# Optimization experiments

Hardware: AMD Instinct MI355X
Metric: run time of the kernel (lower is better)

Reference implementation:

```python
import jax, jax.numpy as jnp
import numpy as np

H = 256      # hidden_dim
NH = 8       # num_heads
D = H // NH  # per-head dim
NEG = -(2.0**32) + 1.0
EPS = 1e-5


def setup_inputs() -> dict:
    key = jax.random.key(0)
    ks = jax.random.split(key, 12)
    N, Tq, Tk = 2, 2048, 2048
    s = 1.0 / np.sqrt(H)
    return {
        "Q": jax.random.normal(ks[0], (N, Tq, H), jnp.float32),
        "K": jax.random.normal(ks[1], (N, Tk, H), jnp.float32),
        "V": jax.random.normal(ks[2], (N, Tk, H), jnp.float32),
        "Wq": jax.random.normal(ks[3], (H, H), jnp.float32) * s,
        "bq": jnp.zeros((H,), jnp.float32),
        "Wk": jax.random.normal(ks[4], (H, H), jnp.float32) * s,
        "bk": jnp.zeros((H,), jnp.float32),
        "Wv": jax.random.normal(ks[5], (H, H), jnp.float32) * s,
        "bv": jnp.zeros((H,), jnp.float32),
        "gamma": jnp.ones((H,), jnp.float32),
        "beta": jnp.zeros((H,), jnp.float32),
    }


def _split_heads(x):
    # [N,T,H] -> [h,N,T,D]  (matches torch split(dim=2)+cat(dim=0): head-major)
    N, T, _ = x.shape
    return x.reshape(N, T, NH, D).transpose(2, 0, 1, 3)


def reference(Q, K, V, Wq, bq, Wk, bk, Wv, bv, gamma, beta):
    N, Tq, _ = Q.shape
    Tk = K.shape[1]
    Ql = jax.nn.relu(Q @ Wq + bq)
    Kl = jax.nn.relu(K @ Wk + bk)
    Vl = jax.nn.relu(V @ Wv + bv)
    Qh, Kh, Vh = _split_heads(Ql), _split_heads(Kl), _split_heads(Vl)

    scores = jnp.einsum("hnqd,hnkd->hnqk", Qh, Kh) / jnp.sqrt(jnp.float32(D))
    key_mask = jnp.sign(jnp.abs(K).sum(-1))    # [N,Tk]
    scores = jnp.where(key_mask[None, :, None, :] == 0, NEG, scores)
    attn = jax.nn.softmax(scores / 0.01, axis=-1)
    query_mask = jnp.sign(jnp.abs(Q).sum(-1))  # [N,Tq]
    attn = attn * query_mask[None, :, :, None]  # dropout p=0 -> identity

    ctx = jnp.einsum("hnqk,hnkd->hnqd", attn[..., :-1], Vh[:, :, :-1, :])
    out = ctx.transpose(1, 2, 0, 3).reshape(N, Tq, H)

    mu = out.mean(-1, keepdims=True)
    var = ((out - mu) ** 2).mean(-1, keepdims=True)
    out = (out - mu) / jnp.sqrt(var + EPS) * gamma + beta

    weight = attn.transpose(1, 2, 0, 3).reshape(N, Tq, NH * Tk).mean(-1)
    return out, weight
```

## Files before the change

kernel.cpp:

```cpp
#include <hip/hip_runtime.h>
#include <math.h>

#define H_DIM 256
#define NHEAD 8
#define DHEAD 32
#define NB 2
#define TSEQ 2048
#define LN_EPS 1e-5f

#define QK2_SCALE 25.503486f
#define SPLIT 4
#define TILES_PER (TSEQ / 64 / SPLIT)

typedef _Float16 half8 __attribute__((ext_vector_type(8)));
typedef _Float16 half4t __attribute__((ext_vector_type(4)));
typedef _Float16 half2t __attribute__((ext_vector_type(2)));
typedef float f32x4 __attribute__((ext_vector_type(4)));

__device__ __forceinline__ f32x4 mfma16(half8 a, half8 b, f32x4 c) {
  return __builtin_amdgcn_mfma_f32_16x16x32_f16(a, b, c, 0, 0, 0);
}
__device__ __forceinline__ float exp2fast(float x) {
  return __builtin_amdgcn_exp2f(x);
}
__device__ __forceinline__ half2t pkrtz(float a, float b) {
  return __builtin_bit_cast(half2t, __builtin_amdgcn_cvt_pkrtz(a, b));
}

__global__ __launch_bounds__(256) void mask_kernel(
    const float* __restrict__ Q, const float* __restrict__ K,
    float* __restrict__ qmask, float* __restrict__ kmask) {
  const int wid = threadIdx.x >> 6, lane = threadIdx.x & 63;
  int row = blockIdx.x * 4 + wid;
  const int total_q = NB * TSEQ;
  const float* src;
  float* dst;
  if (row < total_q) { src = Q + (size_t)row * H_DIM; dst = qmask + row; }
  else               { src = K + (size_t)(row - total_q) * H_DIM; dst = kmask + (row - total_q); }
  float4 v = *(const float4*)(src + lane * 4);
  float s = fabsf(v.x) + fabsf(v.y) + fabsf(v.z) + fabsf(v.w);
  #pragma unroll
  for (int off = 32; off > 0; off >>= 1) s += __shfl_xor(s, off);
  if (lane == 0) *dst = (s != 0.0f) ? 1.0f : 0.0f;
}

__global__ __launch_bounds__(256) void prepack_kernel(
    const float* __restrict__ Wq, const float* __restrict__ Wk, const float* __restrict__ Wv,
    const float* __restrict__ kmask,
    half8* __restrict__ WpkHi, half8* __restrict__ WpkLo, half8* __restrict__ AmaskF) {
  if (blockIdx.x >= 96) {
    int slot2 = (blockIdx.x - 96) * 256 + threadIdx.x;
    int n = slot2 >> 12;
    int rem = slot2 & 4095;
    int tile = rem >> 7;
    int c = (rem >> 6) & 1;
    int lane = rem & 63;
    int quad = lane >> 4, l15 = lane & 15;
    half8 am;
    #pragma unroll
    for (int j = 0; j < 8; ++j)
      am[j] = (l15 == 0) ? (_Float16)kmask[(size_t)n * TSEQ + tile * 64 + c * 32 + quad * 8 + j]
                         : (_Float16)0.0f;
    AmaskF[(((size_t)n * 32 + tile) * 2 + c) * 64 + lane] = am;
    return;
  }
  int slot = blockIdx.x * 256 + threadIdx.x;
  int lane = slot & 63;
  int fg = (slot >> 6) & 15;
  int s  = (slot >> 10) & 7;
  int which = slot >> 13;
  const float* W = which == 0 ? Wq : which == 1 ? Wk : Wv;
  int j  = fg * 16 + (lane & 15);
  int kb = s * 32 + (lane >> 4) * 8;
  half8 hi, lo;
  #pragma unroll
  for (int jj = 0; jj < 8; ++jj) {
    float x = W[(size_t)(kb + jj) * H_DIM + j];
    _Float16 h = (_Float16)x;
    hi[jj] = h;
    lo[jj] = (_Float16)(x - (float)h);
  }
  WpkHi[slot] = hi;
  WpkLo[slot] = lo;
}

__global__ __launch_bounds__(256) void proj_kernel(
    const float* __restrict__ Q, const float* __restrict__ K, const float* __restrict__ V,
    const float* __restrict__ bq, const float* __restrict__ bk, const float* __restrict__ bv,
    const half8* __restrict__ WpkHi, const half8* __restrict__ WpkLo,
    const float* __restrict__ kmask,
    half8* __restrict__ Gqhi, half8* __restrict__ Gqlo,
    half8* __restrict__ Gkhi, half8* __restrict__ Gklo, half8* __restrict__ Gv) {
  const int which = blockIdx.z;
  const float* X    = which == 0 ? Q  : which == 1 ? K  : V;
  const float* bias = which == 0 ? bq : which == 1 ? bk : bv;

  __shared__ __align__(16) float T[64 * 68];

  const int tid = threadIdx.x;
  const int w = tid >> 6, lane = tid & 63;
  const int l15 = lane & 15, quad = lane >> 4;
  const int mbase = blockIdx.y * 64;
  const int nfg   = blockIdx.x * 4;
  const int nn   = mbase >> 11;
  const int tile = blockIdx.y & 31;

  half8 ahi[8], alo[8];
  {
    const float* xrow = X + (size_t)(mbase + w * 16 + l15) * H_DIM + quad * 8;
    #pragma unroll
    for (int s = 0; s < 8; ++s) {
      float4 a0 = *(const float4*)(xrow + s * 32);
      float4 a1 = *(const float4*)(xrow + s * 32 + 4);
      float xs[8] = {a0.x, a0.y, a0.z, a0.w, a1.x, a1.y, a1.z, a1.w};
      #pragma unroll
      for (int i = 0; i < 8; ++i) {
        _Float16 h = (_Float16)xs[i];
        ahi[s][i] = h;
        alo[s][i] = (_Float16)(xs[i] - (float)h);
      }
    }
  }

  f32x4 acc[4];
  #pragma unroll
  for (int f = 0; f < 4; ++f) acc[f] = (f32x4){0.f, 0.f, 0.f, 0.f};

  #pragma unroll
  for (int s = 0; s < 8; ++s) {
    const half8* ph = WpkHi + (((size_t)which * 8 + s) * 16 + nfg) * 64 + lane;
    const half8* pl = WpkLo + (((size_t)which * 8 + s) * 16 + nfg) * 64 + lane;
    #pragma unroll
    for (int f = 0; f < 4; ++f) {
      half8 BH = ph[f * 64];
      half8 BL = pl[f * 64];
      acc[f] = mfma16(ahi[s], BH, acc[f]);
      acc[f] = mfma16(ahi[s], BL, acc[f]);
      acc[f] = mfma16(alo[s], BH, acc[f]);
    }
  }

  #pragma unroll
  for (int f = 0; f < 4; ++f) {
    float bj = bias[blockIdx.x * 64 + f * 16 + l15];
    #pragma unroll
    for (int r = 0; r < 4; ++r) {
      int row = w * 16 + quad * 4 + r;
      float val = fmaxf(acc[f][r] + bj, 0.0f);
      if (which == 2 && ((mbase + row) & (TSEQ - 1)) == TSEQ - 1) val = 0.0f;
      T[row * 68 + f * 16 + l15] = val;
    }
  }
  __syncthreads();

  if (which < 2) {
    const int fq = tid >> 6, lp = tid & 63;
    const int kdc = lp >> 4, krlo = lp & 15;
    const int row = fq * 16 + krlo;
    const float sc = (which == 0) ? QK2_SCALE : 1.0f;
    #pragma unroll
    for (int hs = 0; hs < 2; ++hs) {
      const float* p = &T[row * 68 + hs * 32 + kdc * 8];
      float4 a0 = *(const float4*)p;
      float4 a1 = *(const float4*)(p + 4);
      float xs[8] = {a0.x, a0.y, a0.z, a0.w, a1.x, a1.y, a1.z, a1.w};
      half8 hi, lo;
      #pragma unroll
      for (int i = 0; i < 8; ++i) {
        float x = xs[i] * sc;
        _Float16 h = (_Float16)x;
        hi[i] = h;
        lo[i] = (_Float16)(x - (float)h);
      }
      int hn = (blockIdx.x * 2 + hs) * NB + nn;
      size_t di = ((size_t)hn * 32 + tile) * 256 + tid;
      if (which == 0) { Gqhi[di] = hi; Gqlo[di] = lo; }
      else            { Gkhi[di] = hi; Gklo[di] = lo; }
    }
  } else {
    const int top = tid >> 6, mid = (tid >> 4) & 3, low = tid & 15;
    const int c = top >> 1, hh = top & 1;
    const int trow0 = (c * 4 + mid) * 8;
    float km[8];
    #pragma unroll
    for (int j = 0; j < 8; ++j)
      km[j] = kmask[(size_t)nn * TSEQ + tile * 64 + trow0 + j];
    #pragma unroll
    for (int hs = 0; hs < 2; ++hs) {
      const int col = hs * 32 + hh * 16 + low;
      half8 v8;
      #pragma unroll
      for (int j = 0; j < 8; ++j)
        v8[j] = (_Float16)(T[(trow0 + j) * 68 + col] * km[j]);
      int hn = (blockIdx.x * 2 + hs) * NB + nn;
      Gv[((size_t)hn * 32 + tile) * 256 + tid] = v8;
    }
  }
}

__global__ __launch_bounds__(256) void attn_kernel(
    const half8* __restrict__ Gqhi, const half8* __restrict__ Gqlo,
    const half8* __restrict__ Gkhi, const half8* __restrict__ Gklo,
    const half8* __restrict__ Gv, const half8* __restrict__ AmaskF,
    _Float16* __restrict__ Opf, float* __restrict__ Mp, float* __restrict__ Lp) {
  __shared__ __align__(16) half8 Vf[2][256];
  __shared__ __align__(16) _Float16 Pbuf[4][16][72];

  const int tid = threadIdx.x;
  const int w = tid >> 6, lane = tid & 63;
  const int l15 = lane & 15, quad = lane >> 4;

  const int b = blockIdx.x;
  const int g    = ((b & 7) << 1) | ((b >> 3) & 1);
  const int qt   = (b >> 4) & 31;
  const int sblk = b >> 9;
  const int n = g & 1;

  const size_t fbase = (size_t)g * 32 * 256;
  const int tile0 = sblk * TILES_PER;

  half8 qhi = Gqhi[fbase + (size_t)qt * 256 + w * 64 + lane];
  half8 qlo = Gqlo[fbase + (size_t)qt * 256 + w * 64 + lane];

  float m_q = -1.0e30f;
  f32x4 O0, O1, Ol;
  O0 = (f32x4){0.f, 0.f, 0.f, 0.f};
  O1 = (f32x4){0.f, 0.f, 0.f, 0.f};
  Ol = (f32x4){0.f, 0.f, 0.f, 0.f};

  const half8* kh  = Gkhi + fbase + (size_t)tile0 * 256 + lane;
  const half8* kl  = Gklo + fbase + (size_t)tile0 * 256 + lane;
  const half8* gv  = Gv   + fbase + (size_t)tile0 * 256 + tid;
  const half8* amp = AmaskF + (((size_t)n * 32 + tile0) * 2) * 64 + lane;

  half8 KH[4], KL[4];
  #pragma unroll
  for (int f = 0; f < 4; ++f) { KH[f] = kh[f * 64]; KL[f] = kl[f * 64]; }
  Vf[0][tid] = gv[0];

  #pragma unroll
  for (int tt = 0; tt < TILES_PER; ++tt) {
    half8 KHn[4], KLn[4], vnext;
    if (tt < TILES_PER - 1) {
      #pragma unroll
      for (int f = 0; f < 4; ++f) { KHn[f] = kh[256 + f * 64]; KLn[f] = kl[256 + f * 64]; }
      vnext = gv[256];
    }
    half8 am0 = amp[0];
    half8 am1 = amp[64];

    __syncthreads();
    if (tt < TILES_PER - 1)
      Vf[(tt + 1) & 1][tid] = vnext;

    f32x4 S[4];
    #pragma unroll
    for (int f = 0; f < 4; ++f) {
      f32x4 a = (f32x4){0.f, 0.f, 0.f, 0.f};
      a = mfma16(KL[f], qhi, a);
      a = mfma16(KH[f], qlo, a);
      a = mfma16(KH[f], qhi, a);
      S[f] = a;
    }

    float t0 = fmaxf(fmaxf(S[0][0], S[0][1]), fmaxf(S[0][2], S[0][3]));
    float t1 = fmaxf(fmaxf(S[1][0], S[1][1]), fmaxf(S[1][2], S[1][3]));
    float t2 = fmaxf(fmaxf(S[2][0], S[2][1]), fmaxf(S[2][2], S[2][3]));
    float t3 = fmaxf(fmaxf(S[3][0], S[3][1]), fmaxf(S[3][2], S[3][3]));
    float mx = fmaxf(fmaxf(t0, t1), fmaxf(t2, t3));
    mx = fmaxf(mx, __shfl_xor(mx, 16));
    mx = fmaxf(mx, __shfl_xor(mx, 32));

    float mnew = fmaxf(m_q, mx);
    float alpha = exp2fast(m_q - mnew);
    m_q = mnew;

    #pragma unroll
    for (int f = 0; f < 4; ++f) {
      float p0 = exp2fast(S[f][0] - m_q);
      float p1 = exp2fast(S[f][1] - m_q);
      float p2 = exp2fast(S[f][2] - m_q);
      float p3 = exp2fast(S[f][3] - m_q);
      half2t a01 = pkrtz(p0, p1);
      half2t a23 = pkrtz(p2, p3);
      *(half2t*)&Pbuf[w][l15][f * 16 + quad * 4]     = a01;
      *(half2t*)&Pbuf[w][l15][f * 16 + quad * 4 + 2] = a23;
    }
    #pragma unroll
    for (int r = 0; r < 4; ++r) { O0[r] *= alpha; O1[r] *= alpha; }
    Ol[0] *= alpha;
    asm volatile("s_waitcnt lgkmcnt(0)" ::: "memory");

    const half8* vbuf = (const half8*)Vf[tt & 1];
    #pragma unroll
    for (int c = 0; c < 2; ++c) {
      half8 pb = *(const half8*)&Pbuf[w][l15][c * 32 + quad * 8];
      O0 = mfma16(vbuf[(c * 2 + 0) * 64 + lane], pb, O0);
      O1 = mfma16(vbuf[(c * 2 + 1) * 64 + lane], pb, O1);
      Ol = mfma16(c == 0 ? am0 : am1, pb, Ol);
    }

    #pragma unroll
    for (int f = 0; f < 4; ++f) { KH[f] = KHn[f]; KL[f] = KLn[f]; }
    kh += 256; kl += 256; gv += 256; amp += 128;
  }

  {
    int q = qt * 64 + w * 16 + l15;
    size_t idx = ((size_t)(sblk * 16 + g) * TSEQ + q) * DHEAD;
    half4t o0 = {(_Float16)O0[0], (_Float16)O0[1], (_Float16)O0[2], (_Float16)O0[3]};
    half4t o1 = {(_Float16)O1[0], (_Float16)O1[1], (_Float16)O1[2], (_Float16)O1[3]};
    *(half4t*)&Opf[idx + quad * 4]      = o0;
    *(half4t*)&Opf[idx + 16 + quad * 4] = o1;
    if (quad == 0) {
      Mp[(size_t)(sblk * 16 + g) * TSEQ + q] = m_q;
      Lp[(size_t)(sblk * 16 + g) * TSEQ + q] = Ol[0];
    }
  }
}

__global__ __launch_bounds__(256) void ln_kernel(
    const _Float16* __restrict__ Opf, const float* __restrict__ Mp, const float* __restrict__ Lp,
    const float* __restrict__ gamma, const float* __restrict__ beta,
    const float* __restrict__ qmask,
    float* __restrict__ out, float* __restrict__ wout) {
  const int wid = threadIdx.x >> 6, lane = threadIdx.x & 63;
  const int row = blockIdx.x * 4 + wid;
  const int n = row >> 11, q = row & (TSEQ - 1);
  const int hh = lane >> 3;
  const int hn = hh * NB + n;
  const int dbase = (lane & 7) * 4;

  float m[SPLIT], l[SPLIT];
  half4t P[SPLIT];
  #pragma unroll
  for (int i = 0; i < SPLIT; ++i) {
    size_t si = (size_t)(i * 16 + hn) * TSEQ + q;
    P[i] = *(const half4t*)&Opf[si * DHEAD + dbase];
    m[i] = Mp[si];
    l[i] = Lp[si];
  }
  float mm = fmaxf(fmaxf(m[0], m[1]), fmaxf(m[2], m[3]));
  float denom = 0.f;
  float a[SPLIT];
  #pragma unroll
  for (int i = 0; i < SPLIT; ++i) { a[i] = exp2fast(m[i] - mm); denom += l[i] * a[i]; }
  float qm = qmask[row];
  float inv = qm / denom;

  float4 x = make_float4(0.f, 0.f, 0.f, 0.f);
  #pragma unroll
  for (int i = 0; i < SPLIT; ++i) {
    x.x += (float)P[i][0] * a[i]; x.y += (float)P[i][1] * a[i];
    x.z += (float)P[i][2] * a[i]; x.w += (float)P[i][3] * a[i];
  }
  x.x *= inv; x.y *= inv; x.z *= inv; x.w *= inv;

  float s = x.x + x.y + x.z + x.w;
  #pragma unroll
  for (int off = 32; off > 0; off >>= 1) s += __shfl_xor(s, off);
  float mu = s * (1.0f / H_DIM);
  float dx0 = x.x - mu, dx1 = x.y - mu, dx2 = x.z - mu, dx3 = x.w - mu;
  float sq = dx0 * dx0 + dx1 * dx1 + dx2 * dx2 + dx3 * dx3;
  #pragma unroll
  for (int off = 32; off > 0; off >>= 1) sq += __shfl_xor(sq, off);
  float rstd = rsqrtf(sq * (1.0f / H_DIM) + LN_EPS);
  float4 g = *(const float4*)(gamma + lane * 4);
  float4 bb = *(const float4*)(beta + lane * 4);
  float4 y;
  y.x = dx0 * rstd * g.x + bb.x;
  y.y = dx1 * rstd * g.y + bb.y;
  y.z = dx2 * rstd * g.z + bb.z;
  y.w = dx3 * rstd * g.w + bb.w;
  *(float4*)(out + (size_t)row * H_DIM + lane * 4) = y;
  if (lane == 0) wout[row] = qm * (1.0f / TSEQ);
}

extern "C" void kernel_launch(void* const* d_in, const int* in_sizes, int n_in,
                              void* d_out, int out_size, void* d_ws, size_t ws_size,
                              hipStream_t stream) {
  const float* Q  = (const float*)d_in[0];
  const float* K  = (const float*)d_in[1];
  const float* V  = (const float*)d_in[2];
  const float* Wq = (const float*)d_in[3];
  const float* bq = (const float*)d_in[4];
  const float* Wk = (const float*)d_in[5];
  const float* bk = (const float*)d_in[6];
  const float* Wv = (const float*)d_in[7];
  const float* bv = (const float*)d_in[8];
  const float* gamma = (const float*)d_in[9];
  const float* beta  = (const float*)d_in[10];

  char* ws = (char*)d_ws;
  const size_t NFRAG = (size_t)16 * 32 * 256;
  _Float16* Opf = (_Float16*)ws;
  half8* Gqhi = (half8*)(ws + (size_t)SPLIT * 16 * TSEQ * DHEAD * 2);
  half8* Gqlo = Gqhi + NFRAG;
  half8* Gkhi = Gqlo + NFRAG;
  half8* Gklo = Gkhi + NFRAG;
  half8* Gv   = Gklo + NFRAG;
  float* Mp = (float*)(Gv + NFRAG);
  float* Lp = Mp + SPLIT * 16 * TSEQ;
  float* qmask = Lp + SPLIT * 16 * TSEQ;
  float* kmask = qmask + NB * TSEQ;
  half8* WpkHi = (half8*)(kmask + NB * TSEQ);
  half8* WpkLo = WpkHi + 24576;
  half8* AmaskF = WpkLo + 24576;

  float* out  = (float*)d_out;
  float* wout = out + (size_t)NB * TSEQ * H_DIM;

  hipLaunchKernelGGL(mask_kernel, dim3(2 * NB * TSEQ / 4), dim3(256), 0, stream,
                     Q, K, qmask, kmask);
  hipLaunchKernelGGL(prepack_kernel, dim3(128), dim3(256), 0, stream,
                     Wq, Wk, Wv, kmask, WpkHi, WpkLo, AmaskF);
  hipLaunchKernelGGL(proj_kernel, dim3(H_DIM / 64, NB * TSEQ / 64, 3), dim3(256), 0, stream,
                     Q, K, V, bq, bk, bv, WpkHi, WpkLo, kmask,
                     Gqhi, Gqlo, Gkhi, Gklo, Gv);
  hipLaunchKernelGGL(attn_kernel, dim3(16 * 32 * SPLIT), dim3(256), 0, stream,
                     Gqhi, Gqlo, Gkhi, Gklo, Gv, AmaskF, Opf, Mp, Lp);
  hipLaunchKernelGGL(ln_kernel, dim3(NB * TSEQ / 4), dim3(256), 0, stream,
                     Opf, Mp, Lp, gamma, beta, qmask, out, wout);
}
```

Before: 131.5 us.

## Stage K/V/mask tiles through shared memory and fuse setup kernels

In the attention kernel, each wave used to load the K hi/lo fragments directly from global memory, and all four waves fetched the same data. Now the block cooperatively loads K hi/lo, V and the mask fragment into double-buffered shared memory, with one sync per tile, so each global fetch is shared. The mask and weight-prepack kernels are merged into one setup kernel, and the AmaskF construction moves into the K projection blocks, which removes a launch. It also adds a launch-bounds occupancy hint and a single packed half4 store for P. The trade-off is more LDS reads per tile and a larger shared-memory footprint.

Result: faster. 127.0 us (-3.4%).

```diff
diff --git a/kernel.cpp b/kernel.cpp
--- a/kernel.cpp
+++ b/kernel.cpp
@@ -27,44 +27,28 @@
   return __builtin_bit_cast(half2t, __builtin_amdgcn_cvt_pkrtz(a, b));
 }
 
-__global__ __launch_bounds__(256) void mask_kernel(
+__global__ __launch_bounds__(256) void setup_kernel(
     const float* __restrict__ Q, const float* __restrict__ K,
-    float* __restrict__ qmask, float* __restrict__ kmask) {
-  const int wid = threadIdx.x >> 6, lane = threadIdx.x & 63;
-  int row = blockIdx.x * 4 + wid;
-  const int total_q = NB * TSEQ;
-  const float* src;
-  float* dst;
-  if (row < total_q) { src = Q + (size_t)row * H_DIM; dst = qmask + row; }
-  else               { src = K + (size_t)(row - total_q) * H_DIM; dst = kmask + (row - total_q); }
-  float4 v = *(const float4*)(src + lane * 4);
-  float s = fabsf(v.x) + fabsf(v.y) + fabsf(v.z) + fabsf(v.w);
-  #pragma unroll
-  for (int off = 32; off > 0; off >>= 1) s += __shfl_xor(s, off);
-  if (lane == 0) *dst = (s != 0.0f) ? 1.0f : 0.0f;
-}
-
-__global__ __launch_bounds__(256) void prepack_kernel(
     const float* __restrict__ Wq, const float* __restrict__ Wk, const float* __restrict__ Wv,
-    const float* __restrict__ kmask,
-    half8* __restrict__ WpkHi, half8* __restrict__ WpkLo, half8* __restrict__ AmaskF) {
-  if (blockIdx.x >= 96) {
-    int slot2 = (blockIdx.x - 96) * 256 + threadIdx.x;
-    int n = slot2 >> 12;
-    int rem = slot2 & 4095;
-    int tile = rem >> 7;
-    int c = (rem >> 6) & 1;
-    int lane = rem & 63;
-    int quad = lane >> 4, l15 = lane & 15;
-    half8 am;
-    #pragma unroll
-    for (int j = 0; j < 8; ++j)
-      am[j] = (l15 == 0) ? (_Float16)kmask[(size_t)n * TSEQ + tile * 64 + c * 32 + quad * 8 + j]
-                         : (_Float16)0.0f;
-    AmaskF[(((size_t)n * 32 + tile) * 2 + c) * 64 + lane] = am;
+    float* __restrict__ qmask, float* __restrict__ kmask,
+    half8* __restrict__ WpkHi, half8* __restrict__ WpkLo) {
+  const int tid = threadIdx.x;
+  if (blockIdx.x < 2048) {
+    const int wid = tid >> 6, lane = tid & 63;
+    int row = blockIdx.x * 4 + wid;
+    const int total_q = NB * TSEQ;
+    const float* src;
+    float* dst;
+    if (row < total_q) { src = Q + (size_t)row * H_DIM; dst = qmask + row; }
+    else               { src = K + (size_t)(row - total_q) * H_DIM; dst = kmask + (row - total_q); }
+    float4 v = *(const float4*)(src + lane * 4);
+    float s = fabsf(v.x) + fabsf(v.y) + fabsf(v.z) + fabsf(v.w);
+    #pragma unroll
+    for (int off = 32; off > 0; off >>= 1) s += __shfl_xor(s, off);
+    if (lane == 0) *dst = (s != 0.0f) ? 1.0f : 0.0f;
     return;
   }
-  int slot = blockIdx.x * 256 + threadIdx.x;
+  int slot = (blockIdx.x - 2048) * 256 + tid;
   int lane = slot & 63;
   int fg = (slot >> 6) & 15;
   int s  = (slot >> 10) & 7;
@@ -90,7 +74,8 @@
     const half8* __restrict__ WpkHi, const half8* __restrict__ WpkLo,
     const float* __restrict__ kmask,
     half8* __restrict__ Gqhi, half8* __restrict__ Gqlo,
-    half8* __restrict__ Gkhi, half8* __restrict__ Gklo, half8* __restrict__ Gv) {
+    half8* __restrict__ Gkhi, half8* __restrict__ Gklo, half8* __restrict__ Gv,
+    half8* __restrict__ AmaskF) {
   const int which = blockIdx.z;
   const float* X    = which == 0 ? Q  : which == 1 ? K  : V;
   const float* bias = which == 0 ? bq : which == 1 ? bk : bv;
@@ -177,6 +162,16 @@
       if (which == 0) { Gqhi[di] = hi; Gqlo[di] = lo; }
       else            { Gkhi[di] = hi; Gklo[di] = lo; }
     }
+    if (which == 1 && blockIdx.x == 0 && tid < 128) {
+      int c = tid >> 6, lane2 = tid & 63;
+      int quad2 = lane2 >> 4, l15b = lane2 & 15;
+      half8 am;
+      #pragma unroll
+      for (int j = 0; j < 8; ++j)
+        am[j] = (l15b == 0) ? (_Float16)kmask[(size_t)nn * TSEQ + tile * 64 + c * 32 + quad2 * 8 + j]
+                            : (_Float16)0.0f;
+      AmaskF[(((size_t)nn * 32 + tile) * 2 + c) * 64 + lane2] = am;
+    }
   } else {
     const int top = tid >> 6, mid = (tid >> 4) & 3, low = tid & 15;
     const int c = top >> 1, hh = top & 1;
@@ -198,12 +193,15 @@
   }
 }
 
-__global__ __launch_bounds__(256) void attn_kernel(
+__global__ __launch_bounds__(256, 4) void attn_kernel(
     const half8* __restrict__ Gqhi, const half8* __restrict__ Gqlo,
     const half8* __restrict__ Gkhi, const half8* __restrict__ Gklo,
     const half8* __restrict__ Gv, const half8* __restrict__ AmaskF,
     _Float16* __restrict__ Opf, float* __restrict__ Mp, float* __restrict__ Lp) {
-  __shared__ __align__(16) half8 Vf[2][256];
+  __shared__ __align__(16) half8 KhB[2][256];
+  __shared__ __align__(16) half8 KlB[2][256];
+  __shared__ __align__(16) half8 VB[2][256];
+  __shared__ __align__(16) half8 AB[2][128];
   __shared__ __align__(16) _Float16 Pbuf[4][16][72];
 
   const int tid = threadIdx.x;
@@ -228,38 +226,37 @@
   O1 = (f32x4){0.f, 0.f, 0.f, 0.f};
   Ol = (f32x4){0.f, 0.f, 0.f, 0.f};
 
-  const half8* kh  = Gkhi + fbase + (size_t)tile0 * 256 + lane;
-  const half8* kl  = Gklo + fbase + (size_t)tile0 * 256 + lane;
-  const half8* gv  = Gv   + fbase + (size_t)tile0 * 256 + tid;
-  const half8* amp = AmaskF + (((size_t)n * 32 + tile0) * 2) * 64 + lane;
-
-  half8 KH[4], KL[4];
-  #pragma unroll
-  for (int f = 0; f < 4; ++f) { KH[f] = kh[f * 64]; KL[f] = kl[f * 64]; }
-  Vf[0][tid] = gv[0];
+  const half8* gkh = Gkhi + fbase + (size_t)tile0 * 256;
+  const half8* gkl = Gklo + fbase + (size_t)tile0 * 256;
+  const half8* gvv = Gv   + fbase + (size_t)tile0 * 256;
+  const half8* gam = AmaskF + (size_t)(n * 32 + tile0) * 128;
+
+  KhB[0][tid] = gkh[tid];
+  KlB[0][tid] = gkl[tid];
+  VB[0][tid]  = gvv[tid];
+  if (tid < 128) AB[0][tid] = gam[tid];
+  __syncthreads();
 
   #pragma unroll
   for (int tt = 0; tt < TILES_PER; ++tt) {
-    half8 KHn[4], KLn[4], vnext;
+    const int cur = tt & 1, nxt = cur ^ 1;
+    half8 rkh, rkl, rv, ra;
     if (tt < TILES_PER - 1) {
-      #pragma unroll
-      for (int f = 0; f < 4; ++f) { KHn[f] = kh[256 + f * 64]; KLn[f] = kl[256 + f * 64]; }
-      vnext = gv[256];
-    }
-    half8 am0 = amp[0];
-    half8 am1 = amp[64];
-
-    __syncthreads();
-    if (tt < TILES_PER - 1)
-      Vf[(tt + 1) & 1][tid] = vnext;
+      rkh = gkh[(tt + 1) * 256 + tid];
+      rkl = gkl[(tt + 1) * 256 + tid];
+      rv  = gvv[(tt + 1) * 256 + tid];
+      if (tid < 128) ra = gam[(tt + 1) * 128 + tid];
+    }
 
     f32x4 S[4];
     #pragma unroll
     for (int f = 0; f < 4; ++f) {
+      half8 KH = KhB[cur][f * 64 + lane];
+      half8 KL = KlB[cur][f * 64 + lane];
       f32x4 a = (f32x4){0.f, 0.f, 0.f, 0.f};
-      a = mfma16(KL[f], qhi, a);
-      a = mfma16(KH[f], qlo, a);
-      a = mfma16(KH[f], qhi, a);
+      a = mfma16(KL, qhi, a);
+      a = mfma16(KH, qlo, a);
+      a = mfma16(KH, qhi, a);
       S[f] = a;
     }
 
@@ -283,15 +280,18 @@
       float p3 = exp2fast(S[f][3] - m_q);
       half2t a01 = pkrtz(p0, p1);
       half2t a23 = pkrtz(p2, p3);
-      *(half2t*)&Pbuf[w][l15][f * 16 + quad * 4]     = a01;
-      *(half2t*)&Pbuf[w][l15][f * 16 + quad * 4 + 2] = a23;
+      half4t pk4;
+      pk4[0] = a01[0]; pk4[1] = a01[1]; pk4[2] = a23[0]; pk4[3] = a23[1];
+      *(half4t*)&Pbuf[w][l15][f * 16 + quad * 4] = pk4;
     }
     #pragma unroll
     for (int r = 0; r < 4; ++r) { O0[r] *= alpha; O1[r] *= alpha; }
     Ol[0] *= alpha;
     asm volatile("s_waitcnt lgkmcnt(0)" ::: "memory");
 
-    const half8* vbuf = (const half8*)Vf[tt & 1];
+    half8 am0 = AB[cur][lane];
+    half8 am1 = AB[cur][64 + lane];
+    const half8* vbuf = (const half8*)VB[cur];
     #pragma unroll
     for (int c = 0; c < 2; ++c) {
       half8 pb = *(const half8*)&Pbuf[w][l15][c * 32 + quad * 8];
@@ -300,9 +300,13 @@
       Ol = mfma16(c == 0 ? am0 : am1, pb, Ol);
     }
 
-    #pragma unroll
-    for (int f = 0; f < 4; ++f) { KH[f] = KHn[f]; KL[f] = KLn[f]; }
-    kh += 256; kl += 256; gv += 256; amp += 128;
+    if (tt < TILES_PER - 1) {
+      KhB[nxt][tid] = rkh;
+      KlB[nxt][tid] = rkl;
+      VB[nxt][tid]  = rv;
+      if (tid < 128) AB[nxt][tid] = ra;
+    }
+    __syncthreads();
   }
 
   {
@@ -410,13 +414,11 @@
   float* out  = (float*)d_out;
   float* wout = out + (size_t)NB * TSEQ * H_DIM;
 
-  hipLaunchKernelGGL(mask_kernel, dim3(2 * NB * TSEQ / 4), dim3(256), 0, stream,
-                     Q, K, qmask, kmask);
-  hipLaunchKernelGGL(prepack_kernel, dim3(128), dim3(256), 0, stream,
-                     Wq, Wk, Wv, kmask, WpkHi, WpkLo, AmaskF);
+  hipLaunchKernelGGL(setup_kernel, dim3(2048 + 96), dim3(256), 0, stream,
+                     Q, K, Wq, Wk, Wv, qmask, kmask, WpkHi, WpkLo);
   hipLaunchKernelGGL(proj_kernel, dim3(H_DIM / 64, NB * TSEQ / 64, 3), dim3(256), 0, stream,
                      Q, K, V, bq, bk, bv, WpkHi, WpkLo, kmask,
-                     Gqhi, Gqlo, Gkhi, Gklo, Gv);
+                     Gqhi, Gqlo, Gkhi, Gklo, Gv, AmaskF);
   hipLaunchKernelGGL(attn_kernel, dim3(16 * 32 * SPLIT), dim3(256), 0, stream,
                      Gqhi, Gqlo, Gkhi, Gklo, Gv, AmaskF, Opf, Mp, Lp);
   hipLaunchKernelGGL(ln_kernel, dim3(NB * TSEQ / 4), dim3(256), 0, stream,
```
